# Kernel tuning notes

Measured on AMD Instinct MI355X. Metric: run time of the kernel, lower is better.

Reference implementation:

```python
import jax, jax.numpy as jnp
import numpy as np

N, E, D, H, HEADS_C, G = 50000, 800000, 128, 4, 32, 8
EDIM = D + 2  # H_update: phys_term (D) + ortho_geom (2)


def setup_inputs() -> dict:
    key = jax.random.key(0)
    ks = jax.random.split(key, 24)
    def gl(k, shape, fan_in):
        return jax.random.normal(k, shape, jnp.float32) / np.sqrt(fan_in)
    inp = {
        'h_target': jax.random.normal(ks[0], (N, D), jnp.float32),
        'h_source': jax.random.normal(ks[1], (N, D), jnp.float32),
        'edge_index': jax.random.randint(ks[2], (2, E), 0, N, jnp.int64),
        'pos': jax.random.uniform(ks[3], (N, 2), jnp.float32),
        't_emb': jax.random.normal(ks[4], (1, D), jnp.float32),
        # AdaGN params
        'gn_w': jnp.ones((D,), jnp.float32),
        'gn_b': jnp.zeros((D,), jnp.float32),
        'fc_W': gl(ks[5], (D, 2 * D), D),
        'fc_b': jnp.zeros((2 * D,), jnp.float32),
        # GATv2 params (lin_l, lin_r, lin_edge, att, bias)
        'Wl': gl(ks[6], (D, D), D),
        'bl': jnp.zeros((D,), jnp.float32),
        'Wr': gl(ks[7], (D, D), D),
        'br': jnp.zeros((D,), jnp.float32),
        'We': gl(ks[8], (EDIM, D), EDIM),
        'att': gl(ks[9], (H, HEADS_C), HEADS_C),
        'gat_b': jnp.zeros((D,), jnp.float32),
        # post_gat
        'Wp': gl(ks[10], (D, D), D),
        'bp': jnp.zeros((D,), jnp.float32),
        # update_mlp: LayerNorm + Linear(D,2D) + GELU + Linear(2D,D)
        'ln_w': jnp.ones((D,), jnp.float32),
        'ln_b': jnp.zeros((D,), jnp.float32),
        'W1': gl(ks[11], (D, 2 * D), D),
        'b1': jnp.zeros((2 * D,), jnp.float32),
        'W2': gl(ks[12], (2 * D, D), 2 * D),
        'b2': jnp.zeros((D,), jnp.float32),
    }
    return inp


def _adagn(x, cond, gn_w, gn_b, fc_W, fc_b):
    n, d = x.shape
    xg = x.reshape(n, G, d // G)
    mu = xg.mean(-1, keepdims=True)
    var = xg.var(-1, keepdims=True)  # biased, as torch GroupNorm
    normed = ((xg - mu) / jnp.sqrt(var + 1e-5)).reshape(n, d) * gn_w + gn_b
    style = cond @ fc_W + fc_b  # (1, 2D) broadcasts over nodes
    gamma, beta = jnp.split(style, 2, axis=-1)
    return normed * (1 + gamma) + beta


def _gatv2(h, edge_attr, src, dst, Wl, bl, Wr, br, We, att, gat_b):
    n = h.shape[0]
    x_l = (h @ Wl + bl).reshape(n, H, HEADS_C)  # source transform
    x_r = (h @ Wr + br).reshape(n, H, HEADS_C)  # target transform
    e_feat = (edge_attr @ We).reshape(-1, H, HEADS_C)
    x = x_l[src] + x_r[dst] + e_feat            # (E, H, C)
    x = jax.nn.leaky_relu(x, 0.2)
    logit = jnp.einsum('ehc,hc->eh', x, att)    # (E, H)
    # segment softmax over edges grouped by destination node
    amax = jax.ops.segment_max(logit, dst, num_segments=n)
    amax = jnp.where(jnp.isfinite(amax), amax, 0.0)
    ex = jnp.exp(logit - amax[dst])
    denom = jax.ops.segment_sum(ex, dst, num_segments=n)
    alpha = ex / (denom[dst] + 1e-16)           # (E, H)
    msg = x_l[src] * alpha[:, :, None]          # (E, H, C)
    out = jax.ops.segment_sum(msg, dst, num_segments=n)  # (N, H, C)
    return out.reshape(n, H * HEADS_C) + gat_b


def reference(h_target, h_source, edge_index, pos, t_emb,
              gn_w, gn_b, fc_W, fc_b,
              Wl, bl, Wr, br, We, att, gat_b,
              Wp, bp, ln_w, ln_b, W1, b1, W2, b2):
    h_mod = _adagn(h_source, t_emb, gn_w, gn_b, fc_W, fc_b)
    src, dst = edge_index[0], edge_index[1]
    rel_pos = pos[src] - pos[dst]                       # (E, 2)
    dist_sq = (rel_pos ** 2).sum(-1, keepdims=True) + 1e-8
    geom = rel_pos / dist_sq
    phys = h_mod[src] - h_mod[dst]                      # H_update mode
    ortho = jnp.stack([-geom[:, 1], geom[:, 0]], axis=-1)
    edge_attr = jnp.concatenate([phys, ortho], axis=-1)  # (E, D+2)
    aggr = _gatv2(h_mod, edge_attr, src, dst, Wl, bl, Wr, br, We, att, gat_b)
    aggr = aggr @ Wp + bp
    # update_mlp (dropout inactive in eval)
    mu = aggr.mean(-1, keepdims=True)
    var = aggr.var(-1, keepdims=True)
    z = (aggr - mu) / jnp.sqrt(var + 1e-5) * ln_w + ln_b
    z = jax.nn.gelu(z @ W1 + b1, approximate=False)
    delta = z @ W2 + b2
    return h_target + delta
```

## Files before the change

kernel.cpp:

```cpp
#include <hip/hip_runtime.h>
#include <math.h>

#define D 128
#define LOG2E 1.44269504088896340736f

typedef short bf16x4 __attribute__((ext_vector_type(4)));
typedef short bf16x8 __attribute__((ext_vector_type(8)));
typedef float f32x4  __attribute__((ext_vector_type(4)));
typedef float f32x2  __attribute__((ext_vector_type(2)));

__device__ __forceinline__ float b2f(unsigned short u) {
  union { unsigned int i; float f; } v; v.i = ((unsigned int)u) << 16; return v.f;
}
__device__ __forceinline__ unsigned short f2b(float f) {
  union { float f; unsigned int i; } v; v.f = f;
  unsigned int i = v.i;
  return (unsigned short)((i + 0x7FFFu + ((i >> 16) & 1u)) >> 16);
}
__device__ __forceinline__ float b2f_lo(unsigned int u) {
  union { unsigned int i; float f; } v; v.i = u << 16; return v.f;
}
__device__ __forceinline__ float b2f_hi(unsigned int u) {
  union { unsigned int i; float f; } v; v.i = u & 0xFFFF0000u; return v.f;
}
__device__ __forceinline__ float loadf(const void* p, size_t i, int isb) {
  if (isb) return b2f(((const unsigned short*)p)[i]);
  return ((const float*)p)[i];
}
__device__ __forceinline__ void storeout(void* p, size_t i, float v, int isb) {
  if (isb) ((unsigned short*)p)[i] = f2b(v);
  else     ((float*)p)[i] = v;
}
__device__ __forceinline__ int clampN(int v, int N) {
  return ((unsigned)v >= (unsigned)N) ? 0 : v;
}
__device__ __forceinline__ float gelu_f(float v) {
  return 0.5f * v * (1.f + erff(v * 0.70710678118654752f));
}

__global__ void setup_kernel(const float* __restrict__ gw, const int* __restrict__ e32,
                             int* __restrict__ fflag, int* __restrict__ iflag,
                             int* __restrict__ ok) {
  int t = threadIdx.x;
  if (blockIdx.x == 0) {
    float v = gw[t];
    unsigned long long b = __ballot(v == 1.0f);
    if (t == 0) fflag[0] = (b == 0xFFFFFFFFFFFFFFFFull) ? 0 : 1;
  } else if (blockIdx.x == 1) {
    int v = e32[2 * t + 1];
    unsigned long long b = __ballot(v == 0);
    if (t == 0) iflag[0] = (b == 0xFFFFFFFFFFFFFFFFull) ? 1 : 0;
  } else {
    if (t == 0) ok[0] = 1;
  }
}
__device__ __forceinline__ int edge_src(const void* eraw, int i, int E, int fl, int N) {
  int v = fl ? (int)((const long long*)eraw)[i] : ((const int*)eraw)[i];
  return clampN(v, N);
}
__device__ __forceinline__ int edge_dst(const void* eraw, int i, int E, int fl, int N) {
  int v = fl ? (int)((const long long*)eraw)[(size_t)E + i] : ((const int*)eraw)[(size_t)E + i];
  return clampN(v, N);
}

struct Job { const void* src; float* dst; int n; int blk0; };
struct Jobs { Job j[21]; };
__global__ void cvt_param_kernel(Jobs jobs, const int* __restrict__ fflag, int njobs,
                                 int style_blk,
                                 const void* __restrict__ temb_raw,
                                 const void* __restrict__ fcW_raw,
                                 const void* __restrict__ fcb_raw,
                                 float* __restrict__ style) {
  int isb = fflag[0];
  int b = blockIdx.x;
  if (b == style_blk) {
    int j = threadIdx.x;
    float s = loadf(fcb_raw, j, isb);
    for (int k = 0; k < D; ++k)
      s += loadf(temb_raw, k, isb) * loadf(fcW_raw, (size_t)k * 256 + j, isb);
    style[j] = s;
    return;
  }
  for (int k = 0; k < njobs; ++k) {
    int nblk = (jobs.j[k].n + 255) >> 8;
    int lo = jobs.j[k].blk0;
    if (b >= lo && b < lo + nblk) {
      int i = ((b - lo) << 8) + threadIdx.x;
      if (i < jobs.j[k].n) jobs.j[k].dst[i] = loadf(jobs.j[k].src, i, isb);
      return;
    }
  }
}

__global__ __launch_bounds__(128) void adagn_kernel(
    const void* __restrict__ h_source,
    const float* __restrict__ gn_w, const float* __restrict__ gn_b,
    const float* __restrict__ style, unsigned short* __restrict__ h_mod,
    const int* __restrict__ fflag, int N) {
  int n = blockIdx.x; if (n >= N) return;
  int c = threadIdx.x;
  float x = loadf(h_source, (size_t)n * D + c, fflag[0]);
  float s = x, s2 = x * x;
  s += __shfl_xor(s, 1, 16);  s2 += __shfl_xor(s2, 1, 16);
  s += __shfl_xor(s, 2, 16);  s2 += __shfl_xor(s2, 2, 16);
  s += __shfl_xor(s, 4, 16);  s2 += __shfl_xor(s2, 4, 16);
  s += __shfl_xor(s, 8, 16);  s2 += __shfl_xor(s2, 8, 16);
  float mu = s * (1.f / 16.f);
  float va = s2 * (1.f / 16.f) - mu * mu;
  float iv = rsqrtf(va + 1e-5f);
  float nv = (x - mu) * iv * gn_w[c] + gn_b[c];
  h_mod[(size_t)n * D + c] = f2b(nv * (1.f + style[c]) + style[128 + c]);
}

struct BP { const float* B; int ldb; int col0; };
struct BPJobs { BP j[8]; };
__global__ void bprep_kernel(BPJobs jobs, unsigned short* __restrict__ dst) {
  int job = blockIdx.x >> 7;
  int idx = ((blockIdx.x & 127) << 8) + threadIdx.x;
  int j    = idx & 7;
  int lane = (idx >> 3) & 63;
  int p    = (idx >> 9) & 1;
  int ct   = (idx >> 10) & 7;
  int kt   = idx >> 13;
  int g = lane >> 4;
  int k = kt * 32 + ((j < 4) ? (4 * g + j) : (16 + 4 * g + (j - 4)));
  int n = jobs.j[job].col0 + ct * 16 + (lane & 15);
  float v = jobs.j[job].B[(size_t)k * jobs.j[job].ldb + n];
  unsigned short hi = f2b(v);
  unsigned short out = hi;
  if (p) out = f2b(v - b2f(hi));
  dst[(size_t)job * 32768 + idx] = out;
}

__global__ __launch_bounds__(256) void mgemm3_kernel(
    const unsigned short* __restrict__ A, const unsigned short* __restrict__ Bf,
    const float* __restrict__ bl, const float* __restrict__ br,
    unsigned int* __restrict__ XH32, unsigned short* __restrict__ XR, int Nrows) {
  int l = threadIdx.x & 63, w = threadIdx.x >> 6;
  int rb = blockIdx.x * 64 + w * 16;
  int m = l & 15, g = l >> 4;
  int arow = rb + m;
  if (arow >= Nrows) arow = Nrows - 1;
  const unsigned short* Arow = A + (size_t)arow * 128 + 4 * g;
  f32x4 acc[24];
  #pragma unroll
  for (int ct = 0; ct < 24; ++ct) acc[ct] = (f32x4){0.f, 0.f, 0.f, 0.f};
  #pragma unroll
  for (int kt = 0; kt < 4; ++kt) {
    bf16x4 alo = *(const bf16x4*)(Arow + kt * 32);
    bf16x4 ahi = *(const bf16x4*)(Arow + kt * 32 + 16);
    bf16x8 af = __builtin_shufflevector(alo, ahi, 0, 1, 2, 3, 4, 5, 6, 7);
    #pragma unroll
    for (int ct = 0; ct < 24; ++ct) {
      size_t off = (size_t)(ct >> 3) * 32768 + (size_t)kt * 8192
                 + (size_t)(((ct & 7) * 2) * 64 + l) * 8;
      bf16x8 bh = *(const bf16x8*)(Bf + off);
      bf16x8 bl2 = *(const bf16x8*)(Bf + off + 512);
      acc[ct] = __builtin_amdgcn_mfma_f32_16x16x32_bf16(af, bh, acc[ct], 0, 0, 0);
      acc[ct] = __builtin_amdgcn_mfma_f32_16x16x32_bf16(af, bl2, acc[ct], 0, 0, 0);
    }
  }
  #pragma unroll
  for (int ct = 0; ct < 8; ++ct) {
    int cm = ct * 16 + m;
    #pragma unroll
    for (int r = 0; r < 4; ++r) {
      int row = rb + 4 * g + r;
      if (row < Nrows) {
        float vl = acc[ct][r] + bl[cm];
        float vh = acc[ct + 16][r];
        XH32[(size_t)row * 128 + cm] =
            (unsigned int)f2b(vl) | ((unsigned int)f2b(vh) << 16);
        float vr = acc[ct + 8][r] + br[cm];
        XR[(size_t)row * 128 + cm] = f2b(vr);
      }
    }
  }
}

__global__ void hist_kernel(const void* __restrict__ eraw, const int* __restrict__ iflag,
                            int* __restrict__ deg, int E, int N) {
  int e = blockIdx.x * 256 + threadIdx.x;
  if (e < E) atomicAdd(&deg[edge_dst(eraw, e, E, iflag[0], N)], 1);
}

__global__ __launch_bounds__(1024) void scan1_kernel(const int* __restrict__ deg,
                                                     int* __restrict__ incl,
                                                     int* __restrict__ bsum) {
  int i = blockIdx.x * 1024 + threadIdx.x;
  int lane = threadIdx.x & 63, wave = threadIdx.x >> 6;
  int x = deg[i];
  #pragma unroll
  for (int d = 1; d < 64; d <<= 1) { int t = __shfl_up(x, d, 64); if (lane >= d) x += t; }
  __shared__ int wsum[16];
  if (lane == 63) wsum[wave] = x;
  __syncthreads();
  if (threadIdx.x < 16) {
    int w = wsum[threadIdx.x];
    #pragma unroll
    for (int d = 1; d < 16; d <<= 1) { int t = __shfl_up(w, d, 64); if ((int)threadIdx.x >= d) w += t; }
    wsum[threadIdx.x] = w;
  }
  __syncthreads();
  if (wave > 0) x += wsum[wave - 1];
  incl[i] = x;
  if (threadIdx.x == 1023) bsum[blockIdx.x] = x;
}

__global__ void scan2_kernel(const int* __restrict__ bsum, int* __restrict__ bbase, int nb) {
  if (threadIdx.x == 0) {
    int run = 0;
    for (int b = 0; b < nb; ++b) { bbase[b] = run; run += bsum[b]; }
  }
}

__global__ __launch_bounds__(1024) void scan3_kernel(const int* __restrict__ incl,
                                                     const int* __restrict__ deg,
                                                     const int* __restrict__ bbase,
                                                     int* __restrict__ offs,
                                                     int* __restrict__ cursor, int N) {
  int i = blockIdx.x * 1024 + threadIdx.x;
  if (i < N) {
    int o = bbase[blockIdx.x] + incl[i] - deg[i];
    offs[i] = o; cursor[i] = o;
  }
}

__global__ void scatter_kernel(const void* __restrict__ eraw, const int* __restrict__ iflag,
                               int* __restrict__ cursor, int* __restrict__ elist, int E, int N) {
  int e = blockIdx.x * 256 + threadIdx.x;
  if (e < E) {
    int fl = iflag[0];
    int d = edge_dst(eraw, e, E, fl, N);
    int s = edge_src(eraw, e, E, fl, N);
    int p = atomicAdd(&cursor[d], 1);
    elist[p] = s;
  }
}

__global__ void validate_kernel(const int* __restrict__ offs, const int* __restrict__ deg,
                                const int* __restrict__ cursor, const int* __restrict__ elist,
                                int* __restrict__ ok, int N, int E) {
  int i = blockIdx.x * 256 + threadIdx.x;
  bool bad = false;
  if (i < N) bad = bad || (cursor[i] != offs[i] + deg[i]);
  if (i < E) bad = bad || ((unsigned)elist[i] >= (unsigned)N);
  if (i == 0) bad = bad || (offs[N - 1] + deg[N - 1] != E);
  if (bad) atomicAnd(ok, 0);
}
__global__ void fillc_kernel(void* __restrict__ out, float c, const int* __restrict__ fflag, int n) {
  int i = blockIdx.x * 256 + threadIdx.x;
  if (i < n) storeout(out, i, c, fflag[0]);
}

__global__ __launch_bounds__(256) void edge_kernel(
    const unsigned int* __restrict__ XH32, const unsigned short* __restrict__ XR,
    const float* __restrict__ pos, const float* __restrict__ weo,
    const float* __restrict__ att, const float* __restrict__ gat_b,
    const int* __restrict__ offs, const int* __restrict__ deg,
    const int* __restrict__ elist, unsigned short* __restrict__ aggr, int N) {
  int w = threadIdx.x >> 6;
  int l = threadIdx.x & 63;
  int n = blockIdx.x * 2 + (w >> 1);
  int half = w & 1;
  bool valid = (n < N);
  int nn = valid ? n : 0;
  int c0 = 2 * l;
  uint2 hq = *(const uint2*)(XH32 + (size_t)nn * 128 + c0);
  unsigned int uxr = *(const unsigned int*)(XR + (size_t)nn * 128 + c0);
  f32x2 base = (f32x2){ b2f_lo(uxr) - b2f_hi(hq.x), b2f_hi(uxr) - b2f_hi(hq.y) };
  float2 pd = ((const float2*)pos)[nn];
  f32x2 we0v = (f32x2){ weo[c0], weo[c0 + 1] };
  f32x2 we1v = (f32x2){ weo[128 + c0], weo[128 + c0 + 1] };
  f32x2 attv = (f32x2){ att[c0] * LOG2E, att[c0 + 1] * LOG2E };
  int o = 0, dg = 0;
  if (valid) { o = offs[n]; dg = deg[n]; }
  float mx = -3.402823466e38f, den = 0.f;
  f32x2 num = (f32x2){0.f, 0.f};
  if (dg > half) {
    int s = elist[o + half];
    uint2 q = *(const uint2*)(XH32 + (size_t)s * 128 + c0);
    float2 ps = ((const float2*)pos)[s];
    for (int i = half; i < dg; i += 2) {
      int s2 = elist[o + i + 2];
      uint2 q2 = *(const uint2*)(XH32 + (size_t)s2 * 128 + c0);
      float2 p2 = ((const float2*)pos)[s2];
      float rx = ps.x - pd.x, ry = ps.y - pd.y;
      float inv = 1.f / (rx * rx + ry * ry + 1e-8f);
      float gx = -ry * inv, gy = rx * inv;
      f32x2 xl = (f32x2){ b2f_lo(q.x), b2f_lo(q.y) };
      f32x2 hw = (f32x2){ b2f_hi(q.x), b2f_hi(q.y) };
      f32x2 x = (xl + hw) + (base + gx * we0v + gy * we1v);
      f32x2 lx = __builtin_elementwise_max(x, 0.2f * x);
      f32x2 t = lx * attv;
      float y = t.x + t.y;
      y += __shfl_xor(y, 1, 16);
      y += __shfl_xor(y, 2, 16);
      y += __shfl_xor(y, 4, 16);
      y += __shfl_xor(y, 8, 16);
      float d0 = y - mx;
      if (__any(d0 > 11.5417f)) {
        float mn = fmaxf(mx, y);
        float f = exp2f(mx - mn);
        float p = exp2f(y - mn);
        den = den * f + p;
        num = num * f + p * xl;
        mx = mn;
      } else {
        float p = exp2f(d0);
        den += p;
        num += p * xl;
      }
      s = s2; q = q2; ps = p2;
    }
  }
  __shared__ float4 mrg[4][64];
  mrg[w][l] = (float4){mx, den, num.x, num.y};
  __syncthreads();
  float4 oth = mrg[w ^ 1][l];
  float M = fmaxf(mx, oth.x);
  float f1 = exp2f(mx - M), f2 = exp2f(oth.x - M);
  den = den * f1 + oth.y * f2;
  float n0 = num.x * f1 + oth.z * f2;
  float n1 = num.y * f1 + oth.w * f2;
  if (valid && half == 0) {
    float iden = 1.f / (den + 1e-16f);
    unsigned int o0 = f2b(n0 * iden + gat_b[c0]);
    unsigned int o1 = f2b(n1 * iden + gat_b[c0 + 1]);
    *(unsigned int*)(aggr + (size_t)n * D + c0) = o0 | (o1 << 16);
  }
}

__global__ __launch_bounds__(256) void fused_post_kernel(
    const unsigned short* __restrict__ A, const unsigned short* __restrict__ WP8,
    const float* __restrict__ bp, const float* __restrict__ lnw,
    const float* __restrict__ lnb, const float* __restrict__ b1,
    const float* __restrict__ b2, const void* __restrict__ resid,
    void* __restrict__ out, const int* __restrict__ fflag,
    const int* __restrict__ okf, int Nrows) {
  __shared__ __align__(16) unsigned short ldsU[4][16][268];
  int l = threadIdx.x & 63, w = threadIdx.x >> 6;
  int rb = blockIdx.x * 64 + w * 16;
  int m = l & 15, g = l >> 4;
  int arow = rb + m;
  if (arow >= Nrows) arow = Nrows - 1;
  const unsigned short* Arow = A + (size_t)arow * 128 + 4 * g;

  f32x4 acc[8];
  #pragma unroll
  for (int ct = 0; ct < 8; ++ct) acc[ct] = (f32x4){0.f, 0.f, 0.f, 0.f};
  #pragma unroll
  for (int kt = 0; kt < 4; ++kt) {
    bf16x4 alo = *(const bf16x4*)(Arow + kt * 32);
    bf16x4 ahi = *(const bf16x4*)(Arow + kt * 32 + 16);
    bf16x8 af = __builtin_shufflevector(alo, ahi, 0, 1, 2, 3, 4, 5, 6, 7);
    #pragma unroll
    for (int ct = 0; ct < 8; ++ct) {
      size_t off = (size_t)3 * 32768 + (size_t)kt * 8192 + (size_t)((ct * 2) * 64 + l) * 8;
      bf16x8 bh = *(const bf16x8*)(WP8 + off);
      bf16x8 bl2 = *(const bf16x8*)(WP8 + off + 512);
      acc[ct] = __builtin_amdgcn_mfma_f32_16x16x32_bf16(af, bh, acc[ct], 0, 0, 0);
      acc[ct] = __builtin_amdgcn_mfma_f32_16x16x32_bf16(af, bl2, acc[ct], 0, 0, 0);
    }
  }
  #pragma unroll
  for (int ct = 0; ct < 8; ++ct) acc[ct] = acc[ct] + bp[ct * 16 + m];

  f32x4 s1 = (f32x4){0.f, 0.f, 0.f, 0.f}, s2v = (f32x4){0.f, 0.f, 0.f, 0.f};
  #pragma unroll
  for (int ct = 0; ct < 8; ++ct) { s1 += acc[ct]; s2v += acc[ct] * acc[ct]; }
  #pragma unroll
  for (int d = 1; d < 16; d <<= 1) {
    f32x4 t1, t2;
    #pragma unroll
    for (int r = 0; r < 4; ++r) { t1[r] = __shfl_xor(s1[r], d, 16); t2[r] = __shfl_xor(s2v[r], d, 16); }
    s1 += t1; s2v += t2;
  }
  f32x4 mu = s1 * (1.f / 128.f);
  f32x4 iv;
  #pragma unroll
  for (int r = 0; r < 4; ++r) {
    float var = s2v[r] * (1.f / 128.f) - mu[r] * mu[r];
    iv[r] = rsqrtf(fmaxf(var, 0.f) + 1e-5f);
  }
  #pragma unroll
  for (int ct = 0; ct < 8; ++ct) {
    float lw = lnw[ct * 16 + m], lb = lnb[ct * 16 + m];
    #pragma unroll
    for (int r = 0; r < 4; ++r) {
      float z = (acc[ct][r] - mu[r]) * iv[r] * lw + lb;
      ldsU[w][4 * g + r][m + 16 * ct] = f2b(z);
    }
  }

  f32x4 acc2[16];
  #pragma unroll
  for (int ct = 0; ct < 16; ++ct) acc2[ct] = (f32x4){0.f, 0.f, 0.f, 0.f};
  #pragma unroll
  for (int kt = 0; kt < 4; ++kt) {
    bf16x4 alo = *(const bf16x4*)&ldsU[w][m][4 * g + kt * 32];
    bf16x4 ahi = *(const bf16x4*)&ldsU[w][m][4 * g + kt * 32 + 16];
    bf16x8 af = __builtin_shufflevector(alo, ahi, 0, 1, 2, 3, 4, 5, 6, 7);
    #pragma unroll
    for (int ct = 0; ct < 16; ++ct) {
      size_t off = (size_t)(4 + (ct >> 3)) * 32768 + (size_t)kt * 8192
                 + (size_t)(((ct & 7) * 2) * 64 + l) * 8;
      bf16x8 bh = *(const bf16x8*)(WP8 + off);
      bf16x8 bl2 = *(const bf16x8*)(WP8 + off + 512);
      acc2[ct] = __builtin_amdgcn_mfma_f32_16x16x32_bf16(af, bh, acc2[ct], 0, 0, 0);
      acc2[ct] = __builtin_amdgcn_mfma_f32_16x16x32_bf16(af, bl2, acc2[ct], 0, 0, 0);
    }
  }
  #pragma unroll
  for (int ct = 0; ct < 16; ++ct) {
    float bs = b1[ct * 16 + m];
    #pragma unroll
    for (int r = 0; r < 4; ++r) {
      float v = gelu_f(acc2[ct][r] + bs);
      ldsU[w][4 * g + r][ct * 16 + m] = f2b(v);
    }
  }

  f32x4 acc3[8];
  #pragma unroll
  for (int ct = 0; ct < 8; ++ct) acc3[ct] = (f32x4){0.f, 0.f, 0.f, 0.f};
  #pragma unroll
  for (int kt = 0; kt < 8; ++kt) {
    bf16x4 alo = *(const bf16x4*)&ldsU[w][m][4 * g + kt * 32];
    bf16x4 ahi = *(const bf16x4*)&ldsU[w][m][4 * g + kt * 32 + 16];
    bf16x8 af = __builtin_shufflevector(alo, ahi, 0, 1, 2, 3, 4, 5, 6, 7);
    #pragma unroll
    for (int ct = 0; ct < 8; ++ct) {
      size_t off = (size_t)(6 + (kt >> 2)) * 32768 + (size_t)(kt & 3) * 8192
                 + (size_t)((ct * 2) * 64 + l) * 8;
      bf16x8 bh = *(const bf16x8*)(WP8 + off);
      bf16x8 bl2 = *(const bf16x8*)(WP8 + off + 512);
      acc3[ct] = __builtin_amdgcn_mfma_f32_16x16x32_bf16(af, bh, acc3[ct], 0, 0, 0);
      acc3[ct] = __builtin_amdgcn_mfma_f32_16x16x32_bf16(af, bl2, acc3[ct], 0, 0, 0);
    }
  }
  int isb = fflag[0];
  int okv = okf[0];
  #pragma unroll
  for (int ct = 0; ct < 8; ++ct) {
    int c = ct * 16 + m;
    float bs = b2[c];
    #pragma unroll
    for (int r = 0; r < 4; ++r) {
      int row = rb + 4 * g + r;
      if (row < Nrows) {
        float v = acc3[ct][r] + bs;
        size_t oi = (size_t)row * 128 + c;
        v += loadf(resid, oi, isb);
        if (okv == 0) v = 100.0f;
        storeout(out, oi, v, isb);
      }
    }
  }
}

extern "C" void kernel_launch(void* const* d_in, const int* in_sizes, int n_in,
                              void* d_out, int out_size, void* d_ws, size_t ws_size,
                              hipStream_t stream) {
  const void* h_resid  = d_in[0];
  const void* h_modsrc = d_in[1];
  const void* eidx     = d_in[2];
  const int N = in_sizes[0] / D;
  const int E = in_sizes[2] / 2;
  const int outN = N * D;

  char* wp = (char*)d_ws;
  auto alloc = [&](size_t bytes) -> void* {
    void* p = (void*)wp;
    wp += (bytes + 255) & ~(size_t)255;
    return p;
  };
  unsigned short* BA = (unsigned short*)alloc((size_t)N * D * 2);
  unsigned int*  XH32 = (unsigned int*)alloc((size_t)N * D * 4);
  unsigned short* BX = (unsigned short*)alloc((size_t)N * D * 2);
  float* style = (float*)alloc(256 * 4);
  const int nb = (N + 1023) / 1024;
  const int npad = nb * 1024;
  int* fflag  = (int*)alloc(256);
  int* iflag  = (int*)alloc(256);
  int* okflag = (int*)alloc(256);
  int* elist  = (int*)alloc((size_t)(E + 64) * 4);
  int* deg    = (int*)alloc((size_t)npad * 4);
  int* incl   = (int*)alloc((size_t)npad * 4);
  int* bsum   = (int*)alloc((size_t)nb * 4);
  int* bbase  = (int*)alloc((size_t)nb * 4);
  int* offs   = (int*)alloc((size_t)N * 4);
  int* cursor = (int*)alloc((size_t)N * 4);
  float* pos_f  = (float*)alloc((size_t)2 * N * 4);
  float* gnw_f  = (float*)alloc(128 * 4);
  float* gnb_f  = (float*)alloc(128 * 4);
  float* Wl_f   = (float*)alloc(16384 * 4);
  float* bl_f   = (float*)alloc(128 * 4);
  float* Wr_f   = (float*)alloc(16384 * 4);
  float* br_f   = (float*)alloc(128 * 4);
  float* We_f   = (float*)alloc(16640 * 4);
  float* att_f  = (float*)alloc(128 * 4);
  float* gtb_f  = (float*)alloc(128 * 4);
  float* Wp_f   = (float*)alloc(16384 * 4);
  float* bp_f   = (float*)alloc(128 * 4);
  float* lnw_f  = (float*)alloc(128 * 4);
  float* lnb_f  = (float*)alloc(128 * 4);
  float* W1_f   = (float*)alloc(32768 * 4);
  float* b1_f   = (float*)alloc(256 * 4);
  float* W2_f   = (float*)alloc(32768 * 4);
  float* b2_f   = (float*)alloc(128 * 4);
  unsigned short* WP8 = (unsigned short*)alloc(8 * 65536);

  size_t required = (size_t)(wp - (char*)d_ws);
  if (required > ws_size) {
    return;
  }

  (void)hipMemsetAsync(deg, 0, (size_t)npad * 4, stream);
  (void)hipMemsetAsync(elist + E, 0, 64 * 4, stream);

  setup_kernel<<<3, 64, 0, stream>>>((const float*)d_in[5], (const int*)eidx,
                                     fflag, iflag, okflag);

  const int expected[24] = {6400000, 6400000, 1600000, 100000, 128, 128, 128, 32768,
                            256, 16384, 128, 16384, 128, 16640, 128, 128, 16384, 128,
                            128, 128, 32768, 256, 32768, 128};
  int bad = (n_in == 24) ? -1 : 24;
  if (bad < 0) {
    for (int i = 0; i < 24; ++i) {
      if (in_sizes[i] != expected[i]) { bad = i; break; }
    }
  }
  if (bad >= 0) {
    fillc_kernel<<<(outN + 255) / 256, 256, 0, stream>>>(d_out, 20.f + 10.f * bad, fflag, outN);
    return;
  }

  Jobs jobs;
  int jn = 0, blk = 0;
  auto addjob = [&](const void* s, float* dptr, int n) {
    jobs.j[jn] = {s, dptr, n, blk};
    blk += (n + 255) >> 8;
    ++jn;
  };
  addjob(d_in[3],  pos_f,  2 * N);
  addjob(d_in[5],  gnw_f,  128);
  addjob(d_in[6],  gnb_f,  128);
  addjob(d_in[9],  Wl_f,   16384);
  addjob(d_in[10], bl_f,   128);
  addjob(d_in[11], Wr_f,   16384);
  addjob(d_in[12], br_f,   128);
  addjob(d_in[13], We_f,   16640);
  addjob(d_in[14], att_f,  128);
  addjob(d_in[15], gtb_f,  128);
  addjob(d_in[16], Wp_f,   16384);
  addjob(d_in[17], bp_f,   128);
  addjob(d_in[18], lnw_f,  128);
  addjob(d_in[19], lnb_f,  128);
  addjob(d_in[20], W1_f,   32768);
  addjob(d_in[21], b1_f,   256);
  addjob(d_in[22], W2_f,   32768);
  addjob(d_in[23], b2_f,   128);
  cvt_param_kernel<<<blk + 1, 256, 0, stream>>>(jobs, fflag, jn, blk,
                                                d_in[4], d_in[7], d_in[8], style);

  adagn_kernel<<<N, 128, 0, stream>>>(h_modsrc, gnw_f, gnb_f, style, BA, fflag, N);

  BPJobs bj;
  bj.j[0] = {Wl_f, 128, 0};
  bj.j[1] = {Wr_f, 128, 0};
  bj.j[2] = {We_f, 128, 0};
  bj.j[3] = {Wp_f, 128, 0};
  bj.j[4] = {W1_f, 256, 0};
  bj.j[5] = {W1_f, 256, 128};
  bj.j[6] = {W2_f, 128, 0};
  bj.j[7] = {W2_f + 128 * 128, 128, 0};
  bprep_kernel<<<1024, 256, 0, stream>>>(bj, WP8);

  const int mb = (N + 63) / 64;
  mgemm3_kernel<<<mb, 256, 0, stream>>>(BA, WP8, bl_f, br_f, XH32, BX, N);

  hist_kernel<<<(E + 255) / 256, 256, 0, stream>>>(eidx, iflag, deg, E, N);
  scan1_kernel<<<nb, 1024, 0, stream>>>(deg, incl, bsum);
  scan2_kernel<<<1, 64, 0, stream>>>(bsum, bbase, nb);
  scan3_kernel<<<nb, 1024, 0, stream>>>(incl, deg, bbase, offs, cursor, N);
  scatter_kernel<<<(E + 255) / 256, 256, 0, stream>>>(eidx, iflag, cursor, elist, E, N);
  int vmax = (E > N ? E : N);
  validate_kernel<<<(vmax + 255) / 256, 256, 0, stream>>>(offs, deg, cursor, elist, okflag, N, E);

  edge_kernel<<<(N + 1) / 2, 256, 0, stream>>>(XH32, BX, pos_f, We_f + 128 * 128,
                                               att_f, gtb_f, offs, deg, elist, BA, N);

  fused_post_kernel<<<mb, 256, 0, stream>>>(BA, WP8, bp_f, lnw_f, lnb_f, b1_f, b2_f,
                                            h_resid, d_out, fflag, okflag, N);
}
```

Measured before the change: 554.8 us.

## Stage MFMA weight fragments through LDS with register prefetch in node GEMMs

Both node-level GEMM kernels (the lin_l/lin_r/lin_edge projection and the fused post/MLP kernel) now copy each 16 KB k-slice of the pre-packed weight fragments cooperatively into a shared buffer. The next slice is prefetched into registers while MFMAs read the current slice from LDS. Before, every wave re-read the weights from global/L2 on its own. The change cuts redundant global weight traffic per block, but adds two barriers per k-slice, 16 KB of LDS per block (which can lower occupancy), and extra registers for the prefetch.

```diff
diff --git a/kernel.cpp b/kernel.cpp
--- a/kernel.cpp
+++ b/kernel.cpp
@@ -36,6 +36,13 @@
 }
 __device__ __forceinline__ float gelu_f(float v) {
   return 0.5f * v * (1.f + erff(v * 0.70710678118654752f));
+}
+__device__ __forceinline__ void slice_load(const unsigned short* g, int tid, f32x4* r) {
+  const f32x4* gs = (const f32x4*)g;
+  r[0] = gs[tid]; r[1] = gs[tid + 256]; r[2] = gs[tid + 512]; r[3] = gs[tid + 768];
+}
+__device__ __forceinline__ void slice_store(f32x4* lds, int tid, const f32x4* r) {
+  lds[tid] = r[0]; lds[tid + 256] = r[1]; lds[tid + 512] = r[2]; lds[tid + 768] = r[3];
 }
 
 __global__ void setup_kernel(const float* __restrict__ gw, const int* __restrict__ e32,
@@ -136,28 +143,44 @@
     const unsigned short* __restrict__ A, const unsigned short* __restrict__ Bf,
     const float* __restrict__ bl, const float* __restrict__ br,
     unsigned int* __restrict__ XH32, unsigned short* __restrict__ XR, int Nrows) {
-  int l = threadIdx.x & 63, w = threadIdx.x >> 6;
+  __shared__ __align__(16) f32x4 pbuf[1024];
+  int tid = threadIdx.x;
+  int l = tid & 63, w = tid >> 6;
   int rb = blockIdx.x * 64 + w * 16;
   int m = l & 15, g = l >> 4;
   int arow = rb + m;
   if (arow >= Nrows) arow = Nrows - 1;
   const unsigned short* Arow = A + (size_t)arow * 128 + 4 * g;
-  f32x4 acc[24];
-  #pragma unroll
-  for (int ct = 0; ct < 24; ++ct) acc[ct] = (f32x4){0.f, 0.f, 0.f, 0.f};
+  bf16x8 af[4];
   #pragma unroll
   for (int kt = 0; kt < 4; ++kt) {
     bf16x4 alo = *(const bf16x4*)(Arow + kt * 32);
     bf16x4 ahi = *(const bf16x4*)(Arow + kt * 32 + 16);
-    bf16x8 af = __builtin_shufflevector(alo, ahi, 0, 1, 2, 3, 4, 5, 6, 7);
-    #pragma unroll
-    for (int ct = 0; ct < 24; ++ct) {
-      size_t off = (size_t)(ct >> 3) * 32768 + (size_t)kt * 8192
-                 + (size_t)(((ct & 7) * 2) * 64 + l) * 8;
-      bf16x8 bh = *(const bf16x8*)(Bf + off);
-      bf16x8 bl2 = *(const bf16x8*)(Bf + off + 512);
-      acc[ct] = __builtin_amdgcn_mfma_f32_16x16x32_bf16(af, bh, acc[ct], 0, 0, 0);
-      acc[ct] = __builtin_amdgcn_mfma_f32_16x16x32_bf16(af, bl2, acc[ct], 0, 0, 0);
+    af[kt] = __builtin_shufflevector(alo, ahi, 0, 1, 2, 3, 4, 5, 6, 7);
+  }
+  f32x4 acc[24];
+  #pragma unroll
+  for (int ct = 0; ct < 24; ++ct) acc[ct] = (f32x4){0.f, 0.f, 0.f, 0.f};
+  f32x4 pf[4];
+  slice_load(Bf, tid, pf);
+  slice_store(pbuf, tid, pf);
+  __syncthreads();
+  const unsigned short* pb = (const unsigned short*)pbuf;
+  #pragma unroll
+  for (int p = 0; p < 3; ++p) {
+    #pragma unroll
+    for (int kt = 0; kt < 4; ++kt) {
+      int idx = p * 4 + kt;
+      if (idx < 11) slice_load(Bf + (size_t)(idx + 1) * 8192, tid, pf);
+      #pragma unroll
+      for (int c8 = 0; c8 < 8; ++c8) {
+        bf16x8 bh  = *(const bf16x8*)(pb + ((c8 * 2) * 64 + l) * 8);
+        bf16x8 bl2 = *(const bf16x8*)(pb + ((c8 * 2 + 1) * 64 + l) * 8);
+        acc[p * 8 + c8] = __builtin_amdgcn_mfma_f32_16x16x32_bf16(af[kt], bh,  acc[p * 8 + c8], 0, 0, 0);
+        acc[p * 8 + c8] = __builtin_amdgcn_mfma_f32_16x16x32_bf16(af[kt], bl2, acc[p * 8 + c8], 0, 0, 0);
+      }
+      __syncthreads();
+      if (idx < 11) { slice_store(pbuf, tid, pf); __syncthreads(); }
     }
   }
   #pragma unroll
@@ -338,30 +361,43 @@
     const float* __restrict__ b2, const void* __restrict__ resid,
     void* __restrict__ out, const int* __restrict__ fflag,
     const int* __restrict__ okf, int Nrows) {
+  __shared__ __align__(16) f32x4 pbuf[1024];
   __shared__ __align__(16) unsigned short ldsU[4][16][268];
-  int l = threadIdx.x & 63, w = threadIdx.x >> 6;
+  int tid = threadIdx.x;
+  int l = tid & 63, w = tid >> 6;
   int rb = blockIdx.x * 64 + w * 16;
   int m = l & 15, g = l >> 4;
   int arow = rb + m;
   if (arow >= Nrows) arow = Nrows - 1;
   const unsigned short* Arow = A + (size_t)arow * 128 + 4 * g;
-
-  f32x4 acc[8];
-  #pragma unroll
-  for (int ct = 0; ct < 8; ++ct) acc[ct] = (f32x4){0.f, 0.f, 0.f, 0.f};
+  const unsigned short* pb = (const unsigned short*)pbuf;
+
+  bf16x8 af1[4];
   #pragma unroll
   for (int kt = 0; kt < 4; ++kt) {
     bf16x4 alo = *(const bf16x4*)(Arow + kt * 32);
     bf16x4 ahi = *(const bf16x4*)(Arow + kt * 32 + 16);
-    bf16x8 af = __builtin_shufflevector(alo, ahi, 0, 1, 2, 3, 4, 5, 6, 7);
-    #pragma unroll
-    for (int ct = 0; ct < 8; ++ct) {
-      size_t off = (size_t)3 * 32768 + (size_t)kt * 8192 + (size_t)((ct * 2) * 64 + l) * 8;
-      bf16x8 bh = *(const bf16x8*)(WP8 + off);
-      bf16x8 bl2 = *(const bf16x8*)(WP8 + off + 512);
-      acc[ct] = __builtin_amdgcn_mfma_f32_16x16x32_bf16(af, bh, acc[ct], 0, 0, 0);
-      acc[ct] = __builtin_amdgcn_mfma_f32_16x16x32_bf16(af, bl2, acc[ct], 0, 0, 0);
-    }
+    af1[kt] = __builtin_shufflevector(alo, ahi, 0, 1, 2, 3, 4, 5, 6, 7);
+  }
+  f32x4 pf[4];
+  slice_load(WP8 + (size_t)3 * 32768, tid, pf);
+  slice_store(pbuf, tid, pf);
+  __syncthreads();
+  f32x4 acc[8];
+  #pragma unroll
+  for (int ct = 0; ct < 8; ++ct) acc[ct] = (f32x4){0.f, 0.f, 0.f, 0.f};
+  #pragma unroll
+  for (int kt = 0; kt < 4; ++kt) {
+    if (kt < 3) slice_load(WP8 + (size_t)3 * 32768 + (size_t)(kt + 1) * 8192, tid, pf);
+    #pragma unroll
+    for (int c8 = 0; c8 < 8; ++c8) {
+      bf16x8 bh  = *(const bf16x8*)(pb + ((c8 * 2) * 64 + l) * 8);
+      bf16x8 bl2 = *(const bf16x8*)(pb + ((c8 * 2 + 1) * 64 + l) * 8);
+      acc[c8] = __builtin_amdgcn_mfma_f32_16x16x32_bf16(af1[kt], bh,  acc[c8], 0, 0, 0);
+      acc[c8] = __builtin_amdgcn_mfma_f32_16x16x32_bf16(af1[kt], bl2, acc[c8], 0, 0, 0);
+    }
+    __syncthreads();
+    if (kt < 3) { slice_store(pbuf, tid, pf); __syncthreads(); }
   }
   #pragma unroll
   for (int ct = 0; ct < 8; ++ct) acc[ct] = acc[ct] + bp[ct * 16 + m];
@@ -393,51 +429,63 @@
     }
   }
 
+  slice_load(WP8 + (size_t)4 * 32768, tid, pf);
+  slice_store(pbuf, tid, pf);
+  __syncthreads();
   f32x4 acc2[16];
   #pragma unroll
   for (int ct = 0; ct < 16; ++ct) acc2[ct] = (f32x4){0.f, 0.f, 0.f, 0.f};
   #pragma unroll
-  for (int kt = 0; kt < 4; ++kt) {
+  for (int ph = 0; ph < 2; ++ph) {
+    #pragma unroll
+    for (int kt = 0; kt < 4; ++kt) {
+      int idx = ph * 4 + kt;
+      if (idx < 7) slice_load(WP8 + (size_t)4 * 32768 + (size_t)(idx + 1) * 8192, tid, pf);
+      bf16x4 alo = *(const bf16x4*)&ldsU[w][m][4 * g + kt * 32];
+      bf16x4 ahi = *(const bf16x4*)&ldsU[w][m][4 * g + kt * 32 + 16];
+      bf16x8 af = __builtin_shufflevector(alo, ahi, 0, 1, 2, 3, 4, 5, 6, 7);
+      #pragma unroll
+      for (int c8 = 0; c8 < 8; ++c8) {
+        bf16x8 bh  = *(const bf16x8*)(pb + ((c8 * 2) * 64 + l) * 8);
+        bf16x8 bl2 = *(const bf16x8*)(pb + ((c8 * 2 + 1) * 64 + l) * 8);
+        acc2[ph * 8 + c8] = __builtin_amdgcn_mfma_f32_16x16x32_bf16(af, bh,  acc2[ph * 8 + c8], 0, 0, 0);
+        acc2[ph * 8 + c8] = __builtin_amdgcn_mfma_f32_16x16x32_bf16(af, bl2, acc2[ph * 8 + c8], 0, 0, 0);
+      }
+      __syncthreads();
+      if (idx < 7) { slice_store(pbuf, tid, pf); __syncthreads(); }
+    }
+  }
+  #pragma unroll
+  for (int ct = 0; ct < 16; ++ct) {
+    float bs = b1[ct * 16 + m];
+    #pragma unroll
+    for (int r = 0; r < 4; ++r) {
+      float v = gelu_f(acc2[ct][r] + bs);
+      ldsU[w][4 * g + r][ct * 16 + m] = f2b(v);
+    }
+  }
+
+  slice_load(WP8 + (size_t)6 * 32768, tid, pf);
+  slice_store(pbuf, tid, pf);
+  __syncthreads();
+  f32x4 acc3[8];
+  #pragma unroll
+  for (int ct = 0; ct < 8; ++ct) acc3[ct] = (f32x4){0.f, 0.f, 0.f, 0.f};
+  #pragma unroll
+  for (int kt = 0; kt < 8; ++kt) {
+    if (kt < 7) slice_load(WP8 + (size_t)6 * 32768 + (size_t)(kt + 1) * 8192, tid, pf);
     bf16x4 alo = *(const bf16x4*)&ldsU[w][m][4 * g + kt * 32];
     bf16x4 ahi = *(const bf16x4*)&ldsU[w][m][4 * g + kt * 32 + 16];
     bf16x8 af = __builtin_shufflevector(alo, ahi, 0, 1, 2, 3, 4, 5, 6, 7);
     #pragma unroll
-    for (int ct = 0; ct < 16; ++ct) {
-      size_t off = (size_t)(4 + (ct >> 3)) * 32768 + (size_t)kt * 8192
-                 + (size_t)(((ct & 7) * 2) * 64 + l) * 8;
-      bf16x8 bh = *(const bf16x8*)(WP8 + off);
-      bf16x8 bl2 = *(const bf16x8*)(WP8 + off + 512);
-      acc2[ct] = __builtin_amdgcn_mfma_f32_16x16x32_bf16(af, bh, acc2[ct], 0, 0, 0);
-      acc2[ct] = __builtin_amdgcn_mfma_f32_16x16x32_bf16(af, bl2, acc2[ct], 0, 0, 0);
-    }
-  }
-  #pragma unroll
-  for (int ct = 0; ct < 16; ++ct) {
-    float bs = b1[ct * 16 + m];
-    #pragma unroll
-    for (int r = 0; r < 4; ++r) {
-      float v = gelu_f(acc2[ct][r] + bs);
-      ldsU[w][4 * g + r][ct * 16 + m] = f2b(v);
-    }
-  }
-
-  f32x4 acc3[8];
-  #pragma unroll
-  for (int ct = 0; ct < 8; ++ct) acc3[ct] = (f32x4){0.f, 0.f, 0.f, 0.f};
-  #pragma unroll
-  for (int kt = 0; kt < 8; ++kt) {
-    bf16x4 alo = *(const bf16x4*)&ldsU[w][m][4 * g + kt * 32];
-    bf16x4 ahi = *(const bf16x4*)&ldsU[w][m][4 * g + kt * 32 + 16];
-    bf16x8 af = __builtin_shufflevector(alo, ahi, 0, 1, 2, 3, 4, 5, 6, 7);
-    #pragma unroll
-    for (int ct = 0; ct < 8; ++ct) {
-      size_t off = (size_t)(6 + (kt >> 2)) * 32768 + (size_t)(kt & 3) * 8192
-                 + (size_t)((ct * 2) * 64 + l) * 8;
-      bf16x8 bh = *(const bf16x8*)(WP8 + off);
-      bf16x8 bl2 = *(const bf16x8*)(WP8 + off + 512);
-      acc3[ct] = __builtin_amdgcn_mfma_f32_16x16x32_bf16(af, bh, acc3[ct], 0, 0, 0);
-      acc3[ct] = __builtin_amdgcn_mfma_f32_16x16x32_bf16(af, bl2, acc3[ct], 0, 0, 0);
-    }
+    for (int c8 = 0; c8 < 8; ++c8) {
+      bf16x8 bh  = *(const bf16x8*)(pb + ((c8 * 2) * 64 + l) * 8);
+      bf16x8 bl2 = *(const bf16x8*)(pb + ((c8 * 2 + 1) * 64 + l) * 8);
+      acc3[c8] = __builtin_amdgcn_mfma_f32_16x16x32_bf16(af, bh,  acc3[c8], 0, 0, 0);
+      acc3[c8] = __builtin_amdgcn_mfma_f32_16x16x32_bf16(af, bl2, acc3[c8], 0, 0, 0);
+    }
+    __syncthreads();
+    if (kt < 7) { slice_store(pbuf, tid, pf); __syncthreads(); }
   }
   int isb = fflag[0];
   int okv = okf[0];
```

Result: faster. 504.1 us (-9.1%).
